# Kernel optimization log

Hardware: AMD Instinct MI355X
Metric: run time of the kernel (lower is better)

The kernel has to match this reference:

```python
import jax, jax.numpy as jnp
import numpy as np

B, S, E, H = 8, 1024, 512, 16
L = S            # block_len == seq_len (only valid operating point of the module)
D = E // H       # d_head = 32


def setup_inputs() -> dict:
    key = jax.random.key(0)
    k0, k1, k2, k3, k4 = jax.random.split(key, 5)
    scale = 1.0 / np.sqrt(E).astype(np.float32)
    return {
        "x": jax.random.normal(k0, (B, S, E), dtype=jnp.float32),
        "Wq": jax.random.normal(k1, (E, E), dtype=jnp.float32) * scale,  # torch Linear weight (out,in)
        "Wk": jax.random.normal(k2, (E, E), dtype=jnp.float32) * scale,
        "Wv": jax.random.normal(k3, (E, E), dtype=jnp.float32) * scale,
        "Er": jax.random.normal(k4, (2 * L - 1, D), dtype=jnp.float32),  # relative pos embeddings
    }


def reference(x, Wq, Wk, Wv, Er):
    b, s, e = x.shape
    l = s  # block_len == seq_len -> pad_len = 0, n_block = 1
    # projections (torch Linear: y = x @ W.T), split heads -> [b, h, l, d]
    q = (x @ Wq.T).reshape(b, s, H, D).transpose(0, 2, 1, 3)
    k = (x @ Wk.T).reshape(b, s, H, D).transpose(0, 2, 1, 3)
    v = (x @ Wv.T).reshape(b, s, H, D).transpose(0, 2, 1, 3)

    # content scores [b, h, l, l]
    QK = jnp.einsum('bhqd,bhkd->bhqk', q, k)

    # relative position bias. The pad/flatten/reshape skew trick in the original
    # is exactly Srel[i, j] = q[i] . Er[j - i + L - 1] (mask_QEr zeros entries
    # that the skew never reads). Implemented as a gather of Er + einsum.
    rel_idx = jnp.arange(l)[None, :] - jnp.arange(l)[:, None] + (l - 1)  # [l, l] in [0, 2l-2]
    Er_g = Er[rel_idx]                                                   # [l, l, d]
    Srel = jnp.einsum('bhid,ijd->bhij', q, Er_g)

    # NOTE: the module's causal `mask` buffer is never applied in forward.
    attn = jax.nn.softmax((QK + Srel) / np.sqrt(D).astype(np.float32), axis=-1)
    out = jnp.einsum('bhij,bhjd->bhid', attn, v)       # [b, h, l, d]
    out = out.transpose(0, 2, 1, 3).reshape(b, s, e)   # merge heads
    return out  # dropout is identity in eval / p=0
```

## Files before the change

### kernel.cpp

```cpp
#include <hip/hip_runtime.h>
#include <hip/hip_bf16.h>


typedef short bf16x8 __attribute__((ext_vector_type(8)));
typedef float f32x4 __attribute__((ext_vector_type(4)));
typedef unsigned short u16x4 __attribute__((ext_vector_type(4)));
typedef unsigned int u32x4 __attribute__((ext_vector_type(4)));

#if __has_builtin(__builtin_amdgcn_exp2f)
#define EXP2F(x) __builtin_amdgcn_exp2f(x)
#else
#define EXP2F(x) exp2f(x)
#endif

constexpr int Bb = 8, Ss = 1024, Ee = 512, Hh = 16, Dd = 32;
#define QSCALE 0.25503486f

__device__ __forceinline__ bf16x8 ldg_frag(const __hip_bfloat16* p) {
    return *reinterpret_cast<const bf16x8*>(p);
}

__device__ __forceinline__ unsigned short bf16_bits(float v) {
    return __builtin_bit_cast(unsigned short, __float2bfloat16(v));
}

__device__ __forceinline__ unsigned pack_bf16(float lo, float hi) {
    return (unsigned)bf16_bits(lo) | ((unsigned)bf16_bits(hi) << 16);
}

__device__ __forceinline__ float bperm_f(int addr, float v) {
    return __builtin_bit_cast(float,
        __builtin_amdgcn_ds_bpermute(addr, __builtin_bit_cast(int, v)));
}

__global__ __launch_bounds__(256) void convert_kernel(
    const float* __restrict__ x,  const float* __restrict__ wq,
    const float* __restrict__ wk, const float* __restrict__ wv,
    const float* __restrict__ er,
    __hip_bfloat16* __restrict__ xb, __hip_bfloat16* __restrict__ wb,
    __hip_bfloat16* __restrict__ erb)
{
    const int GX = 1048576, GW = 65536, GE = 16376;
    int g = blockIdx.x * 256 + threadIdx.x;
    if (g >= GX + 3 * GW + GE) return;
    const float* src;
    __hip_bfloat16* dst;
    int rel;
    if (g < GX)               { src = x;  dst = xb;          rel = g; }
    else if (g < GX +   GW)   { src = wq; dst = wb;          rel = g - GX; }
    else if (g < GX + 2*GW)   { src = wk; dst = wb + 262144; rel = g - GX - GW; }
    else if (g < GX + 3*GW)   { src = wv; dst = wb + 524288; rel = g - GX - 2*GW; }
    else                      { src = er; dst = erb;         rel = g - GX - 3*GW; }
    const float4 v = *reinterpret_cast<const float4*>(src + (size_t)rel * 4);
    u16x4 pk;
    pk[0] = bf16_bits(v.x);
    pk[1] = bf16_bits(v.y);
    pk[2] = bf16_bits(v.z);
    pk[3] = bf16_bits(v.w);
    *reinterpret_cast<u16x4*>(dst + (size_t)rel * 4) = pk;
}

__global__ __launch_bounds__(256) void proj_kernel(
    const __hip_bfloat16* __restrict__ xb,
    const __hip_bfloat16* __restrict__ wb,
    __hip_bfloat16* __restrict__ Qs,
    __hip_bfloat16* __restrict__ Kh,
    unsigned* __restrict__ Vt32)
{
    const int tid  = threadIdx.x;
    const int wave = tid >> 6;
    const int lane = tid & 63;
    const int li   = lane & 15;
    const int quad = lane >> 4;

    const int m0    = blockIdx.y * 64;
    const int nbase = blockIdx.x * 256 + wave * 64;

    f32x4 acc[4][4];
    #pragma unroll
    for (int rf = 0; rf < 4; ++rf)
        #pragma unroll
        for (int t = 0; t < 4; ++t) acc[rf][t] = f32x4{0.f, 0.f, 0.f, 0.f};

    const __hip_bfloat16* xp = xb + (size_t)(m0 + li) * Ee + quad * 8;
    const __hip_bfloat16* wp = wb + (size_t)(nbase + li) * Ee + quad * 8;

    for (int k0 = 0; k0 < Ee; k0 += 32) {
        bf16x8 a[4], bfr[4];
        #pragma unroll
        for (int rf = 0; rf < 4; ++rf) a[rf]  = ldg_frag(xp + rf * 16 * Ee + k0);
        #pragma unroll
        for (int t = 0; t < 4; ++t)    bfr[t] = ldg_frag(wp + t * 16 * Ee + k0);
        #pragma unroll
        for (int rf = 0; rf < 4; ++rf)
            #pragma unroll
            for (int t = 0; t < 4; ++t)
                acc[rf][t] = __builtin_amdgcn_mfma_f32_16x16x32_bf16(
                    a[rf], bfr[t], acc[rf][t], 0, 0, 0);
    }

    const int mat = nbase >> 9;
    const int nn0 = nbase & 511;
    const int bb  = m0 >> 10;
    const int sb  = m0 & 1023;
    if (mat == 2) {
        #pragma unroll
        for (int t = 0; t < 4; ++t) {
            int nn = nn0 + t * 16 + li;
            int h = nn >> 5, d = nn & 31;
            size_t base = ((size_t)(bb * Hh + h) * Dd + d) * 512
                        + (sb >> 5) * 16 + quad * 4;
            #pragma unroll
            for (int p = 0; p < 2; ++p) {
                u32x4 pk;
                #pragma unroll
                for (int r = 0; r < 4; ++r)
                    pk[r] = pack_bf16(acc[2*p][t][r], acc[2*p+1][t][r]);
                *reinterpret_cast<u32x4*>(Vt32 + base + (size_t)p * 16) = pk;
            }
        }
    } else {
        __hip_bfloat16* dst = (mat == 0) ? Qs : Kh;
        const float sc = (mat == 0) ? QSCALE : 1.0f;
        #pragma unroll
        for (int rf = 0; rf < 4; ++rf) {
            const int srow = sb + rf * 16 + quad * 4;
            #pragma unroll
            for (int t = 0; t < 4; ++t) {
                int nn = nn0 + t * 16 + li;
                int h = nn >> 5, d = nn & 31;
                #pragma unroll
                for (int r = 0; r < 4; ++r)
                    dst[((size_t)(bb * Hh + h) * Ss + (srow + r)) * Dd + d] =
                        __float2bfloat16(acc[rf][t][r] * sc);
            }
        }
    }
}

__global__ __launch_bounds__(256) void attn_kernel(
    const __hip_bfloat16* __restrict__ Qs,
    const __hip_bfloat16* __restrict__ Kh,
    const __hip_bfloat16* __restrict__ Vt,
    const __hip_bfloat16* __restrict__ Er,
    float* __restrict__ out)
{
    const int tid  = threadIdx.x;
    const int wave = tid >> 6;
    const int lane = tid & 63;
    const int li   = lane & 15;
    const int quad = lane >> 4;

    const int c  = blockIdx.x & 127;
    const int b  = c >> 4;
    const int h  = c & 15;
    const int ib = blockIdx.x >> 7;
    const int i0 = ib * 128 + wave * 32;

    const __hip_bfloat16* Qp = Qs + (size_t)(b * Hh + h) * Ss * Dd;
    const __hip_bfloat16* Kp = Kh + (size_t)(b * Hh + h) * Ss * Dd;
    const __hip_bfloat16* Vp = Vt + (size_t)(b * Hh + h) * Dd * Ss;

    __shared__ unsigned pb_lds[4][4][16 * 20];
    unsigned* pbA0 = pb_lds[wave][0];
    unsigned* pbA1 = pb_lds[wave][1];
    unsigned* pbB0 = pb_lds[wave][2];
    unsigned* pbB1 = pb_lds[wave][3];

    const bf16x8 qfA = ldg_frag(Qp + (i0      + li) * Dd + quad * 8);
    const bf16x8 qfB = ldg_frag(Qp + (i0 + 16 + li) * Dd + quad * 8);

    int addr4[4];
    bool cond[4];
    #pragma unroll
    for (int r = 0; r < 4; ++r) {
        const int row = quad * 4 + r;
        addr4[r] = (16 * quad + ((li - row + 15) & 15)) * 4;
        cond[r]  = (li <= row);
    }
    const int pbw = quad * 80 + li;
    const int pbr = li * 20 + quad * 4;

    f32x4 oA0 = f32x4{0,0,0,0}, oA1 = f32x4{0,0,0,0};
    f32x4 oB0 = f32x4{0,0,0,0}, oB1 = f32x4{0,0,0,0};
    float lsumA[4] = {0,0,0,0}, lsumB[4] = {0,0,0,0};
    const f32x4 zero = f32x4{0,0,0,0};

    for (int j0 = 0; j0 < Ss; j0 += 64) {
        bf16x8 k0 = ldg_frag(Kp + (j0      + li) * Dd + quad * 8);
        bf16x8 k1 = ldg_frag(Kp + (j0 + 16 + li) * Dd + quad * 8);
        bf16x8 k2 = ldg_frag(Kp + (j0 + 32 + li) * Dd + quad * 8);
        bf16x8 k3 = ldg_frag(Kp + (j0 + 48 + li) * Dd + quad * 8);
        const int rb = j0 - i0 + 1008;
        bf16x8 em = ldg_frag(Er + (rb - 16 + li) * Dd + quad * 8);
        bf16x8 e0 = ldg_frag(Er + (rb      + li) * Dd + quad * 8);
        bf16x8 e1 = ldg_frag(Er + (rb + 16 + li) * Dd + quad * 8);
        bf16x8 e2 = ldg_frag(Er + (rb + 32 + li) * Dd + quad * 8);
        bf16x8 e3 = ldg_frag(Er + (rb + 48 + li) * Dd + quad * 8);
        bf16x8 e4 = ldg_frag(Er + (rb + 64 + li) * Dd + quad * 8);
        bf16x8 v0 = ldg_frag(Vp + (li     ) * Ss + j0 + quad * 8);
        bf16x8 v1 = ldg_frag(Vp + (li + 16) * Ss + j0 + quad * 8);
        bf16x8 v2 = ldg_frag(Vp + (li     ) * Ss + j0 + 32 + quad * 8);
        bf16x8 v3 = ldg_frag(Vp + (li + 16) * Ss + j0 + 32 + quad * 8);

        {
            f32x4 s0 = __builtin_amdgcn_mfma_f32_16x16x32_bf16(qfA, k0, zero, 0, 0, 0);
            f32x4 s1 = __builtin_amdgcn_mfma_f32_16x16x32_bf16(qfA, k1, zero, 0, 0, 0);
            f32x4 s2 = __builtin_amdgcn_mfma_f32_16x16x32_bf16(qfA, k2, zero, 0, 0, 0);
            f32x4 s3 = __builtin_amdgcn_mfma_f32_16x16x32_bf16(qfA, k3, zero, 0, 0, 0);
            f32x4 q0 = __builtin_amdgcn_mfma_f32_16x16x32_bf16(qfA, e0, zero, 0, 0, 0);
            f32x4 q1 = __builtin_amdgcn_mfma_f32_16x16x32_bf16(qfA, e1, zero, 0, 0, 0);
            f32x4 q2 = __builtin_amdgcn_mfma_f32_16x16x32_bf16(qfA, e2, zero, 0, 0, 0);
            f32x4 q3 = __builtin_amdgcn_mfma_f32_16x16x32_bf16(qfA, e3, zero, 0, 0, 0);
            f32x4 q4 = __builtin_amdgcn_mfma_f32_16x16x32_bf16(qfA, e4, zero, 0, 0, 0);
            float p0[4], p1[4], p2[4], p3[4];
            #pragma unroll
            for (int r = 0; r < 4; ++r) {
                float f0 = bperm_f(addr4[r], q0[r]);
                float f1 = bperm_f(addr4[r], q1[r]);
                float f2 = bperm_f(addr4[r], q2[r]);
                float f3 = bperm_f(addr4[r], q3[r]);
                float f4 = bperm_f(addr4[r], q4[r]);
                p0[r] = EXP2F(s0[r] + (cond[r] ? f0 : f1));
                p1[r] = EXP2F(s1[r] + (cond[r] ? f1 : f2));
                p2[r] = EXP2F(s2[r] + (cond[r] ? f2 : f3));
                p3[r] = EXP2F(s3[r] + (cond[r] ? f3 : f4));
                lsumA[r] += (p0[r] + p1[r]) + (p2[r] + p3[r]);
            }
            #pragma unroll
            for (int r = 0; r < 4; ++r) {
                pbA0[pbw + 20 * r] = pack_bf16(p0[r], p1[r]);
                pbA1[pbw + 20 * r] = pack_bf16(p2[r], p3[r]);
            }
            bf16x8 pf0 = *reinterpret_cast<const bf16x8*>(&pbA0[pbr]);
            bf16x8 pf1 = *reinterpret_cast<const bf16x8*>(&pbA1[pbr]);
            oA0 = __builtin_amdgcn_mfma_f32_16x16x32_bf16(pf0, v0, oA0, 0, 0, 0);
            oA1 = __builtin_amdgcn_mfma_f32_16x16x32_bf16(pf0, v1, oA1, 0, 0, 0);
            oA0 = __builtin_amdgcn_mfma_f32_16x16x32_bf16(pf1, v2, oA0, 0, 0, 0);
            oA1 = __builtin_amdgcn_mfma_f32_16x16x32_bf16(pf1, v3, oA1, 0, 0, 0);
        }

        {
            f32x4 s0 = __builtin_amdgcn_mfma_f32_16x16x32_bf16(qfB, k0, zero, 0, 0, 0);
            f32x4 s1 = __builtin_amdgcn_mfma_f32_16x16x32_bf16(qfB, k1, zero, 0, 0, 0);
            f32x4 s2 = __builtin_amdgcn_mfma_f32_16x16x32_bf16(qfB, k2, zero, 0, 0, 0);
            f32x4 s3 = __builtin_amdgcn_mfma_f32_16x16x32_bf16(qfB, k3, zero, 0, 0, 0);
            f32x4 q0 = __builtin_amdgcn_mfma_f32_16x16x32_bf16(qfB, em, zero, 0, 0, 0);
            f32x4 q1 = __builtin_amdgcn_mfma_f32_16x16x32_bf16(qfB, e0, zero, 0, 0, 0);
            f32x4 q2 = __builtin_amdgcn_mfma_f32_16x16x32_bf16(qfB, e1, zero, 0, 0, 0);
            f32x4 q3 = __builtin_amdgcn_mfma_f32_16x16x32_bf16(qfB, e2, zero, 0, 0, 0);
            f32x4 q4 = __builtin_amdgcn_mfma_f32_16x16x32_bf16(qfB, e3, zero, 0, 0, 0);
            float p0[4], p1[4], p2[4], p3[4];
            #pragma unroll
            for (int r = 0; r < 4; ++r) {
                float f0 = bperm_f(addr4[r], q0[r]);
                float f1 = bperm_f(addr4[r], q1[r]);
                float f2 = bperm_f(addr4[r], q2[r]);
                float f3 = bperm_f(addr4[r], q3[r]);
                float f4 = bperm_f(addr4[r], q4[r]);
                p0[r] = EXP2F(s0[r] + (cond[r] ? f0 : f1));
                p1[r] = EXP2F(s1[r] + (cond[r] ? f1 : f2));
                p2[r] = EXP2F(s2[r] + (cond[r] ? f2 : f3));
                p3[r] = EXP2F(s3[r] + (cond[r] ? f3 : f4));
                lsumB[r] += (p0[r] + p1[r]) + (p2[r] + p3[r]);
            }
            #pragma unroll
            for (int r = 0; r < 4; ++r) {
                pbB0[pbw + 20 * r] = pack_bf16(p0[r], p1[r]);
                pbB1[pbw + 20 * r] = pack_bf16(p2[r], p3[r]);
            }
            bf16x8 pf0 = *reinterpret_cast<const bf16x8*>(&pbB0[pbr]);
            bf16x8 pf1 = *reinterpret_cast<const bf16x8*>(&pbB1[pbr]);
            oB0 = __builtin_amdgcn_mfma_f32_16x16x32_bf16(pf0, v0, oB0, 0, 0, 0);
            oB1 = __builtin_amdgcn_mfma_f32_16x16x32_bf16(pf0, v1, oB1, 0, 0, 0);
            oB0 = __builtin_amdgcn_mfma_f32_16x16x32_bf16(pf1, v2, oB0, 0, 0, 0);
            oB1 = __builtin_amdgcn_mfma_f32_16x16x32_bf16(pf1, v3, oB1, 0, 0, 0);
        }
    }

    #pragma unroll
    for (int r = 0; r < 4; ++r) {
        float va = lsumA[r], vb = lsumB[r];
        va += __shfl_xor(va, 1, 64);  vb += __shfl_xor(vb, 1, 64);
        va += __shfl_xor(va, 2, 64);  vb += __shfl_xor(vb, 2, 64);
        va += __shfl_xor(va, 4, 64);  vb += __shfl_xor(vb, 4, 64);
        va += __shfl_xor(va, 8, 64);  vb += __shfl_xor(vb, 8, 64);
        lsumA[r] = 1.0f / va;
        lsumB[r] = 1.0f / vb;
    }
    #pragma unroll
    for (int r = 0; r < 4; ++r) {
        const int srowA = i0 + quad * 4 + r;
        float* opA = out + ((size_t)b * Ss + srowA) * Ee + h * Dd;
        opA[li]      = oA0[r] * lsumA[r];
        opA[16 + li] = oA1[r] * lsumA[r];
        float* opB = opA + 16 * Ee;
        opB[li]      = oB0[r] * lsumB[r];
        opB[16 + li] = oB1[r] * lsumB[r];
    }
}

extern "C" void kernel_launch(void* const* d_in, const int* in_sizes, int n_in,
                              void* d_out, int out_size, void* d_ws, size_t ws_size,
                              hipStream_t stream) {
    const float* x  = (const float*)d_in[0];
    const float* Wq = (const float*)d_in[1];
    const float* Wk = (const float*)d_in[2];
    const float* Wv = (const float*)d_in[3];
    const float* Er = (const float*)d_in[4];
    float* out = (float*)d_out;

    __hip_bfloat16* xb  = reinterpret_cast<__hip_bfloat16*>(d_ws);
    __hip_bfloat16* wbb = xb  + (size_t)8192 * 512;
    __hip_bfloat16* erb = wbb + (size_t)1536 * 512;
    __hip_bfloat16* Qs  = erb + 65536;
    __hip_bfloat16* Kh  = Qs  + (size_t)Bb * Hh * Ss * Dd;
    __hip_bfloat16* Vt  = Kh  + (size_t)Bb * Hh * Ss * Dd;

    convert_kernel<<<4929, 256, 0, stream>>>(x, Wq, Wk, Wv, Er, xb, wbb, erb);
    proj_kernel<<<dim3(6, 128), 256, 0, stream>>>(
        xb, wbb, Qs, Kh, reinterpret_cast<unsigned*>(Vt));
    attn_kernel<<<dim3(1024), 256, 0, stream>>>(Qs, Kh, Vt, erb, out);
}
```

Baseline: 195.3 us.

## Select before bpermute, compute row sums via MFMA, use packed bf16 convert

The relative-bias path now chooses between neighbouring MFMA outputs before the lane permute, so each row needs four ds_bpermute calls instead of five. The softmax row sum moves from per-lane VALU adds plus a shuffle reduction to extra MFMAs against a vector of ones, which also makes the sum use the same bf16-rounded probabilities as the PV product. Conversions use the packed v_cvt_pk_bf16_f32 instruction in all kernels. s_setprio hints are wrapped around the MFMA blocks. The cost is two extra MFMAs per tile and inline asm that depends on the target ISA.

```diff
diff --git a/kernel.cpp b/kernel.cpp
--- a/kernel.cpp
+++ b/kernel.cpp
@@ -4,7 +4,7 @@
 
 typedef short bf16x8 __attribute__((ext_vector_type(8)));
 typedef float f32x4 __attribute__((ext_vector_type(4)));
-typedef unsigned short u16x4 __attribute__((ext_vector_type(4)));
+typedef unsigned int u32x2 __attribute__((ext_vector_type(2)));
 typedef unsigned int u32x4 __attribute__((ext_vector_type(4)));
 
 #if __has_builtin(__builtin_amdgcn_exp2f)
@@ -20,12 +20,10 @@
     return *reinterpret_cast<const bf16x8*>(p);
 }
 
-__device__ __forceinline__ unsigned short bf16_bits(float v) {
-    return __builtin_bit_cast(unsigned short, __float2bfloat16(v));
-}
-
 __device__ __forceinline__ unsigned pack_bf16(float lo, float hi) {
-    return (unsigned)bf16_bits(lo) | ((unsigned)bf16_bits(hi) << 16);
+    unsigned r;
+    asm("v_cvt_pk_bf16_f32 %0, %1, %2" : "=v"(r) : "v"(lo), "v"(hi));
+    return r;
 }
 
 __device__ __forceinline__ float bperm_f(int addr, float v) {
@@ -52,12 +50,10 @@
     else if (g < GX + 3*GW)   { src = wv; dst = wb + 524288; rel = g - GX - 2*GW; }
     else                      { src = er; dst = erb;         rel = g - GX - 3*GW; }
     const float4 v = *reinterpret_cast<const float4*>(src + (size_t)rel * 4);
-    u16x4 pk;
-    pk[0] = bf16_bits(v.x);
-    pk[1] = bf16_bits(v.y);
-    pk[2] = bf16_bits(v.z);
-    pk[3] = bf16_bits(v.w);
-    *reinterpret_cast<u16x4*>(dst + (size_t)rel * 4) = pk;
+    u32x2 pk;
+    pk[0] = pack_bf16(v.x, v.y);
+    pk[1] = pack_bf16(v.z, v.w);
+    *reinterpret_cast<u32x2*>(dst + (size_t)rel * 4) = pk;
 }
 
 __global__ __launch_bounds__(256) void proj_kernel(
@@ -129,10 +125,16 @@
             for (int t = 0; t < 4; ++t) {
                 int nn = nn0 + t * 16 + li;
                 int h = nn >> 5, d = nn & 31;
+                size_t base = ((size_t)(bb * Hh + h) * Ss + srow) * Dd + d;
                 #pragma unroll
-                for (int r = 0; r < 4; ++r)
-                    dst[((size_t)(bb * Hh + h) * Ss + (srow + r)) * Dd + d] =
-                        __float2bfloat16(acc[rf][t][r] * sc);
+                for (int r = 0; r < 4; r += 2) {
+                    unsigned w = pack_bf16(acc[rf][t][r]     * sc,
+                                           acc[rf][t][r + 1] * sc);
+                    dst[base + (size_t)r * Dd] =
+                        __builtin_bit_cast(__hip_bfloat16, (unsigned short)(w & 0xffffu));
+                    dst[base + (size_t)(r + 1) * Dd] =
+                        __builtin_bit_cast(__hip_bfloat16, (unsigned short)(w >> 16));
+                }
             }
         }
     }
@@ -171,20 +173,24 @@
     const bf16x8 qfB = ldg_frag(Qp + (i0 + 16 + li) * Dd + quad * 8);
 
     int addr4[4];
-    bool cond[4];
+    bool sel[4];
     #pragma unroll
     for (int r = 0; r < 4; ++r) {
         const int row = quad * 4 + r;
         addr4[r] = (16 * quad + ((li - row + 15) & 15)) * 4;
-        cond[r]  = (li <= row);
+        sel[r]   = (li + row >= 15);
     }
     const int pbw = quad * 80 + li;
     const int pbr = li * 20 + quad * 4;
 
     f32x4 oA0 = f32x4{0,0,0,0}, oA1 = f32x4{0,0,0,0};
     f32x4 oB0 = f32x4{0,0,0,0}, oB1 = f32x4{0,0,0,0};
-    float lsumA[4] = {0,0,0,0}, lsumB[4] = {0,0,0,0};
+    f32x4 lsA = f32x4{0,0,0,0}, lsB = f32x4{0,0,0,0};
     const f32x4 zero = f32x4{0,0,0,0};
+
+    bf16x8 ones;
+    #pragma unroll
+    for (int i = 0; i < 8; ++i) ones[i] = (short)0x3F80;
 
     for (int j0 = 0; j0 < Ss; j0 += 64) {
         bf16x8 k0 = ldg_frag(Kp + (j0      + li) * Dd + quad * 8);
@@ -204,6 +210,7 @@
         bf16x8 v3 = ldg_frag(Vp + (li + 16) * Ss + j0 + 32 + quad * 8);
 
         {
+            __builtin_amdgcn_s_setprio(1);
             f32x4 s0 = __builtin_amdgcn_mfma_f32_16x16x32_bf16(qfA, k0, zero, 0, 0, 0);
             f32x4 s1 = __builtin_amdgcn_mfma_f32_16x16x32_bf16(qfA, k1, zero, 0, 0, 0);
             f32x4 s2 = __builtin_amdgcn_mfma_f32_16x16x32_bf16(qfA, k2, zero, 0, 0, 0);
@@ -213,19 +220,18 @@
             f32x4 q2 = __builtin_amdgcn_mfma_f32_16x16x32_bf16(qfA, e2, zero, 0, 0, 0);
             f32x4 q3 = __builtin_amdgcn_mfma_f32_16x16x32_bf16(qfA, e3, zero, 0, 0, 0);
             f32x4 q4 = __builtin_amdgcn_mfma_f32_16x16x32_bf16(qfA, e4, zero, 0, 0, 0);
+            __builtin_amdgcn_s_setprio(0);
             float p0[4], p1[4], p2[4], p3[4];
             #pragma unroll
             for (int r = 0; r < 4; ++r) {
-                float f0 = bperm_f(addr4[r], q0[r]);
-                float f1 = bperm_f(addr4[r], q1[r]);
-                float f2 = bperm_f(addr4[r], q2[r]);
-                float f3 = bperm_f(addr4[r], q3[r]);
-                float f4 = bperm_f(addr4[r], q4[r]);
-                p0[r] = EXP2F(s0[r] + (cond[r] ? f0 : f1));
-                p1[r] = EXP2F(s1[r] + (cond[r] ? f1 : f2));
-                p2[r] = EXP2F(s2[r] + (cond[r] ? f2 : f3));
-                p3[r] = EXP2F(s3[r] + (cond[r] ? f3 : f4));
-                lsumA[r] += (p0[r] + p1[r]) + (p2[r] + p3[r]);
+                float m0 = sel[r] ? q0[r] : q1[r];
+                float m1 = sel[r] ? q1[r] : q2[r];
+                float m2 = sel[r] ? q2[r] : q3[r];
+                float m3 = sel[r] ? q3[r] : q4[r];
+                p0[r] = EXP2F(s0[r] + bperm_f(addr4[r], m0));
+                p1[r] = EXP2F(s1[r] + bperm_f(addr4[r], m1));
+                p2[r] = EXP2F(s2[r] + bperm_f(addr4[r], m2));
+                p3[r] = EXP2F(s3[r] + bperm_f(addr4[r], m3));
             }
             #pragma unroll
             for (int r = 0; r < 4; ++r) {
@@ -234,13 +240,18 @@
             }
             bf16x8 pf0 = *reinterpret_cast<const bf16x8*>(&pbA0[pbr]);
             bf16x8 pf1 = *reinterpret_cast<const bf16x8*>(&pbA1[pbr]);
+            __builtin_amdgcn_s_setprio(1);
             oA0 = __builtin_amdgcn_mfma_f32_16x16x32_bf16(pf0, v0, oA0, 0, 0, 0);
             oA1 = __builtin_amdgcn_mfma_f32_16x16x32_bf16(pf0, v1, oA1, 0, 0, 0);
             oA0 = __builtin_amdgcn_mfma_f32_16x16x32_bf16(pf1, v2, oA0, 0, 0, 0);
             oA1 = __builtin_amdgcn_mfma_f32_16x16x32_bf16(pf1, v3, oA1, 0, 0, 0);
+            lsA = __builtin_amdgcn_mfma_f32_16x16x32_bf16(pf0, ones, lsA, 0, 0, 0);
+            lsA = __builtin_amdgcn_mfma_f32_16x16x32_bf16(pf1, ones, lsA, 0, 0, 0);
+            __builtin_amdgcn_s_setprio(0);
         }
 
         {
+            __builtin_amdgcn_s_setprio(1);
             f32x4 s0 = __builtin_amdgcn_mfma_f32_16x16x32_bf16(qfB, k0, zero, 0, 0, 0);
             f32x4 s1 = __builtin_amdgcn_mfma_f32_16x16x32_bf16(qfB, k1, zero, 0, 0, 0);
             f32x4 s2 = __builtin_amdgcn_mfma_f32_16x16x32_bf16(qfB, k2, zero, 0, 0, 0);
@@ -250,19 +261,18 @@
             f32x4 q2 = __builtin_amdgcn_mfma_f32_16x16x32_bf16(qfB, e1, zero, 0, 0, 0);
             f32x4 q3 = __builtin_amdgcn_mfma_f32_16x16x32_bf16(qfB, e2, zero, 0, 0, 0);
             f32x4 q4 = __builtin_amdgcn_mfma_f32_16x16x32_bf16(qfB, e3, zero, 0, 0, 0);
+            __builtin_amdgcn_s_setprio(0);
             float p0[4], p1[4], p2[4], p3[4];
             #pragma unroll
             for (int r = 0; r < 4; ++r) {
-                float f0 = bperm_f(addr4[r], q0[r]);
-                float f1 = bperm_f(addr4[r], q1[r]);
-                float f2 = bperm_f(addr4[r], q2[r]);
-                float f3 = bperm_f(addr4[r], q3[r]);
-                float f4 = bperm_f(addr4[r], q4[r]);
-                p0[r] = EXP2F(s0[r] + (cond[r] ? f0 : f1));
-                p1[r] = EXP2F(s1[r] + (cond[r] ? f1 : f2));
-                p2[r] = EXP2F(s2[r] + (cond[r] ? f2 : f3));
-                p3[r] = EXP2F(s3[r] + (cond[r] ? f3 : f4));
-                lsumB[r] += (p0[r] + p1[r]) + (p2[r] + p3[r]);
+                float m0 = sel[r] ? q0[r] : q1[r];
+                float m1 = sel[r] ? q1[r] : q2[r];
+                float m2 = sel[r] ? q2[r] : q3[r];
+                float m3 = sel[r] ? q3[r] : q4[r];
+                p0[r] = EXP2F(s0[r] + bperm_f(addr4[r], m0));
+                p1[r] = EXP2F(s1[r] + bperm_f(addr4[r], m1));
+                p2[r] = EXP2F(s2[r] + bperm_f(addr4[r], m2));
+                p3[r] = EXP2F(s3[r] + bperm_f(addr4[r], m3));
             }
             #pragma unroll
             for (int r = 0; r < 4; ++r) {
@@ -271,32 +281,31 @@
             }
             bf16x8 pf0 = *reinterpret_cast<const bf16x8*>(&pbB0[pbr]);
             bf16x8 pf1 = *reinterpret_cast<const bf16x8*>(&pbB1[pbr]);
+            __builtin_amdgcn_s_setprio(1);
             oB0 = __builtin_amdgcn_mfma_f32_16x16x32_bf16(pf0, v0, oB0, 0, 0, 0);
             oB1 = __builtin_amdgcn_mfma_f32_16x16x32_bf16(pf0, v1, oB1, 0, 0, 0);
             oB0 = __builtin_amdgcn_mfma_f32_16x16x32_bf16(pf1, v2, oB0, 0, 0, 0);
             oB1 = __builtin_amdgcn_mfma_f32_16x16x32_bf16(pf1, v3, oB1, 0, 0, 0);
+            lsB = __builtin_amdgcn_mfma_f32_16x16x32_bf16(pf0, ones, lsB, 0, 0, 0);
+            lsB = __builtin_amdgcn_mfma_f32_16x16x32_bf16(pf1, ones, lsB, 0, 0, 0);
+            __builtin_amdgcn_s_setprio(0);
         }
     }
 
     #pragma unroll
     for (int r = 0; r < 4; ++r) {
-        float va = lsumA[r], vb = lsumB[r];
-        va += __shfl_xor(va, 1, 64);  vb += __shfl_xor(vb, 1, 64);
-        va += __shfl_xor(va, 2, 64);  vb += __shfl_xor(vb, 2, 64);
-        va += __shfl_xor(va, 4, 64);  vb += __shfl_xor(vb, 4, 64);
-        va += __shfl_xor(va, 8, 64);  vb += __shfl_xor(vb, 8, 64);
-        lsumA[r] = 1.0f / va;
-        lsumB[r] = 1.0f / vb;
+        lsA[r] = 1.0f / lsA[r];
+        lsB[r] = 1.0f / lsB[r];
     }
     #pragma unroll
     for (int r = 0; r < 4; ++r) {
         const int srowA = i0 + quad * 4 + r;
         float* opA = out + ((size_t)b * Ss + srowA) * Ee + h * Dd;
-        opA[li]      = oA0[r] * lsumA[r];
-        opA[16 + li] = oA1[r] * lsumA[r];
+        opA[li]      = oA0[r] * lsA[r];
+        opA[16 + li] = oA1[r] * lsA[r];
         float* opB = opA + 16 * Ee;
-        opB[li]      = oB0[r] * lsumB[r];
-        opB[16 + li] = oB1[r] * lsumB[r];
+        opB[li]      = oB0[r] * lsB[r];
+        opB[16 + li] = oB1[r] * lsB[r];
     }
 }
 
```

After: 208.4 us. 1.07x slower.
